# Performance work log

Measured on AMD Instinct MI355X. Metric: run time of the kernel, lower is better.

The kernel has to match this reference:

```python
import jax, jax.numpy as jnp
import numpy as np

B, S, H = 2, 2048, 1024
NUM_HEADS = 16


def setup_inputs() -> dict:
    key = jax.random.key(0)
    ks = jax.random.split(key, 5)
    scale = 1.0 / np.sqrt(H)
    x = jax.random.normal(ks[0], (B, S, H), dtype=jnp.float32)
    W_qkv = jax.random.normal(ks[1], (3 * H, H), dtype=jnp.float32) * scale
    b_qkv = jax.random.normal(ks[2], (3 * H,), dtype=jnp.float32) * 0.02
    W_o = jax.random.normal(ks[3], (H, H), dtype=jnp.float32) * scale
    b_o = jax.random.normal(ks[4], (H,), dtype=jnp.float32) * 0.02
    return {"x": x, "W_qkv": W_qkv, "b_qkv": b_qkv, "W_o": W_o, "b_o": b_o}


def reference(x, W_qkv, b_qkv, W_o, b_o):
    b, s, h = x.shape
    n = NUM_HEADS
    d_head = h // n
    # QKV projection (torch Linear: x @ W.T + b), then chunk into Q, K, V
    qkv = x @ W_qkv.T + b_qkv                      # [b, s, 3h]
    Q, K, V = jnp.split(qkv, 3, axis=-1)           # each [b, s, h]
    # split heads: b s (n d) -> b n s d
    Q = Q.reshape(b, s, n, d_head).transpose(0, 2, 1, 3)
    K = K.reshape(b, s, n, d_head).transpose(0, 2, 1, 3)
    V = V.reshape(b, s, n, d_head).transpose(0, 2, 1, 3)
    # scores, causal mask, scale (mask before/after scale is equivalent: -inf stays -inf)
    scores = jnp.einsum('bnqd,bnkd->bnqk', Q, K) / jnp.sqrt(jnp.float32(d_head))
    causal = jnp.tril(jnp.ones((s, s), dtype=bool))  # True = keep
    scores = jnp.where(causal, scores, -jnp.inf)
    A = jax.nn.softmax(scores, axis=-1)
    AV = jnp.einsum('bnqk,bnkd->bnqd', A, V)
    out = AV.transpose(0, 2, 1, 3).reshape(b, s, h)  # merge heads
    return out @ W_o.T + b_o
```

## Files before the change

kernel.cpp:

```cpp
#include <hip/hip_runtime.h>
#include <cstdint>
#include <cstddef>

#define BATCH 2
#define SEQ   2048
#define HID   1024
#define NHEAD 16
#define DHEAD 64
#define QKV_N 3072
#define NTOK  4096

typedef __attribute__((ext_vector_type(4))) float f32x4;
typedef __attribute__((ext_vector_type(8))) short bf16x8;

#define QSCL 0.18033688011112042f

__device__ inline unsigned short f2bf(float f) {
    union { float f; unsigned int u; } v; v.f = f;
    unsigned int u = v.u;
    unsigned int r = (u + 0x7fffu + ((u >> 16) & 1u)) >> 16;
    return (unsigned short)r;
}

__device__ __forceinline__ unsigned int pack_bf16_rh(float a, float b) {
    union { float f; unsigned int u; } ua, ub;
    ua.f = a; ub.f = b;
    return ((ua.u + 0x8000u) >> 16) | ((ub.u + 0x8000u) & 0xffff0000u);
}

__device__ __forceinline__ void gload_lds16(const void* g, void* l) {
    __builtin_amdgcn_global_load_lds(
        (const __attribute__((address_space(1))) void*)g,
        (__attribute__((address_space(3))) void*)l, 16, 0, 0);
}

__global__ void cast_f32_bf16(const float* __restrict__ in, unsigned short* __restrict__ out, int n4) {
    int i = blockIdx.x * blockDim.x + threadIdx.x;
    if (i >= n4) return;
    float4 v = reinterpret_cast<const float4*>(in)[i];
    ushort4 o;
    o.x = f2bf(v.x); o.y = f2bf(v.y); o.z = f2bf(v.z); o.w = f2bf(v.w);
    reinterpret_cast<ushort4*>(out)[i] = o;
}

template<int BN, int OUT_MODE>
__global__ __launch_bounds__(256) void gemm_bt(const short* __restrict__ A,
                                               const short* __restrict__ B,
                                               const float* __restrict__ bias,
                                               void* __restrict__ Cout,
                                               int M, int N, int K) {
    constexpr int WTN = BN / 2;
    constexpr int NJ  = WTN / 16;
    constexpr int NBC = BN / 64;

    __shared__ short sA[2][128 * 32];
    __shared__ short sB[2][BN * 32];

    const int tid  = threadIdx.x;
    const int lane = tid & 63;
    const int wave = tid >> 6;
    const int wm = wave >> 1, wn = wave & 1;

    const int nwg = gridDim.x;
    const int swz = (blockIdx.x & 7) * (nwg >> 3) + (blockIdx.x >> 3);
    const int tiles_n = N / BN;
    const int m0 = (swz / tiles_n) * 128;
    const int n0 = (swz % tiles_n) * BN;

    f32x4 acc[4][NJ];
    #pragma unroll
    for (int i = 0; i < 4; ++i)
        #pragma unroll
        for (int j = 0; j < NJ; ++j) acc[i][j] = (f32x4){0.f, 0.f, 0.f, 0.f};

    const int r = lane & 15;
    const int G = lane >> 4;

    #define GSTAGE(kt_, buf_)                                                          \
        {                                                                              \
            _Pragma("unroll")                                                          \
            for (int i = 0; i < 2; ++i) {                                              \
                int ga = (i * 4 + wave) * 64 + lane;                                   \
                int row = ga >> 2, gcol = (ga & 3) ^ (row & 3);                        \
                gload_lds16(A + (size_t)(m0 + row) * K + (kt_) + gcol * 8,             \
                            &sA[buf_][(i * 4 + wave) * 512]);                          \
            }                                                                          \
            _Pragma("unroll")                                                          \
            for (int i = 0; i < NBC; ++i) {                                            \
                int gb = (i * 4 + wave) * 64 + lane;                                   \
                int row = gb >> 2, gcol = (gb & 3) ^ (row & 3);                        \
                gload_lds16(B + (size_t)(n0 + row) * K + (kt_) + gcol * 8,             \
                            &sB[buf_][(i * 4 + wave) * 512]);                          \
            }                                                                          \
        }

    GSTAGE(0, 0);
    __syncthreads();
    int cur = 0;

    const int nsteps = K >> 5;
    for (int ks = 0; ks < nsteps; ++ks) {
        if (ks + 1 < nsteps) GSTAGE((ks + 1) * 32, cur ^ 1);

        const int sg = G ^ (r & 3);
        bf16x8 af[4], bfr[NJ];
        #pragma unroll
        for (int i = 0; i < 4; ++i) {
            int row = wm * 64 + i * 16 + r;
            af[i] = *reinterpret_cast<const bf16x8*>(&sA[cur][row * 32 + sg * 8]);
        }
        #pragma unroll
        for (int j = 0; j < NJ; ++j) {
            int row = wn * WTN + j * 16 + r;
            bfr[j] = *reinterpret_cast<const bf16x8*>(&sB[cur][row * 32 + sg * 8]);
        }
        #pragma unroll
        for (int i = 0; i < 4; ++i)
            #pragma unroll
            for (int j = 0; j < NJ; ++j)
                acc[i][j] = __builtin_amdgcn_mfma_f32_16x16x32_bf16(af[i], bfr[j], acc[i][j], 0, 0, 0);

        __syncthreads();
        cur ^= 1;
    }
    #undef GSTAGE

    const int col_l = lane & 15;
    const int row_g = (lane >> 4) * 4;
    #pragma unroll
    for (int i = 0; i < 4; ++i) {
        #pragma unroll
        for (int j = 0; j < NJ; ++j) {
            int nn = n0 + wn * WTN + j * 16 + col_l;
            float bv = bias[nn];
            float scl = (OUT_MODE == 2 && nn < HID) ? QSCL : 1.0f;
            #pragma unroll
            for (int reg = 0; reg < 4; ++reg) {
                int mm = m0 + wm * 64 + i * 16 + row_g + reg;
                float v = (acc[i][j][reg] + bv) * scl;
                if (OUT_MODE == 0) {
                    reinterpret_cast<float*>(Cout)[(size_t)mm * N + nn] = v;
                } else {
                    reinterpret_cast<unsigned short*>(Cout)[(size_t)mm * N + nn] = f2bf(v);
                }
            }
        }
    }
}

#define TLDP 72
__global__ __launch_bounds__(256) void transpose_v(const short* __restrict__ qkv,
                                                   short* __restrict__ vP) {
    const int st = blockIdx.x;
    const int bh = blockIdx.y;
    const int b  = bh >> 4, h = bh & 15;
    __shared__ short ld[64 * TLDP];
    const int tid = threadIdx.x;

    #pragma unroll
    for (int i = 0; i < 2; ++i) {
        int idx = i * 256 + tid;
        int row = idx >> 3, c = idx & 7;
        int4 v = *reinterpret_cast<const int4*>(
            qkv + ((size_t)(b * SEQ + st * 64 + row)) * QKV_N + 2 * HID + h * DHEAD + c * 8);
        *reinterpret_cast<int4*>(&ld[row * TLDP + c * 8]) = v;
    }
    __syncthreads();
    #pragma unroll
    for (int i = 0; i < 2; ++i) {
        int u  = i * 256 + tid;
        int Tp = u >> 8;
        int d  = (u >> 2) & 63;
        int p  = u & 3;
        int b0 = Tp * 32 + 4 * p;
        int b1 = b0 + 16;
        ushort4 o0, o1;
        o0.x = (unsigned short)ld[(b0 + 0) * TLDP + d];
        o0.y = (unsigned short)ld[(b0 + 1) * TLDP + d];
        o0.z = (unsigned short)ld[(b0 + 2) * TLDP + d];
        o0.w = (unsigned short)ld[(b0 + 3) * TLDP + d];
        o1.x = (unsigned short)ld[(b1 + 0) * TLDP + d];
        o1.y = (unsigned short)ld[(b1 + 1) * TLDP + d];
        o1.z = (unsigned short)ld[(b1 + 2) * TLDP + d];
        o1.w = (unsigned short)ld[(b1 + 3) * TLDP + d];
        size_t out = ((size_t)((bh * 64 + st * 2 + Tp) * 64 + d)) * 32 + p * 8;
        *reinterpret_cast<ushort4*>(&vP[out])     = o0;
        *reinterpret_cast<ushort4*>(&vP[out + 4]) = o1;
    }
}

__global__ __launch_bounds__(256) void attn_fwd(const short* __restrict__ qkv,
                                                const short* __restrict__ vP,
                                                short* __restrict__ av) {
    const int bid = blockIdx.x;
    const int qb  = 31 - (bid >> 5);
    const int bh  = bid & 31;
    const int b   = bh >> 4;
    const int h   = bh & 15;

    __shared__ float comb[64][68];

    const int tid  = threadIdx.x;
    const int lane = tid & 63;
    const int wave = tid >> 6;
    const int r    = lane & 15;
    const int G    = lane >> 4;
    const int row_g = G * 4;

    const int qbw = qb * 64;

    bf16x8 qf[4][2];
    #pragma unroll
    for (int mi = 0; mi < 4; ++mi) {
        const short* Qg = qkv + ((size_t)(b * SEQ + qbw + mi * 16 + r)) * QKV_N + h * DHEAD;
        qf[mi][0] = *reinterpret_cast<const bf16x8*>(Qg + G * 8);
        qf[mi][1] = *reinterpret_cast<const bf16x8*>(Qg + 32 + G * 8);
    }

    f32x4 oacc[4][4];
    f32x4 oL[4];
    #pragma unroll
    for (int mi = 0; mi < 4; ++mi) {
        oL[mi] = (f32x4){0.f, 0.f, 0.f, 0.f};
        #pragma unroll
        for (int dg = 0; dg < 4; ++dg) oacc[mi][dg] = (f32x4){0.f, 0.f, 0.f, 0.f};
    }

    bf16x8 ones;
    #pragma unroll
    for (int e = 0; e < 8; ++e) ones[e] = (short)0x3f80;

    const short* kpt = qkv + (size_t)(b * SEQ + wave * 32) * QKV_N + HID + h * DHEAD
                       + r * QKV_N + G * 8;
    const short* vpt = vP + (size_t)(bh * 64 + wave) * 2048 + r * 32 + G * 8;
    const ptrdiff_t KSTEP = (ptrdiff_t)128 * QKV_N;
    const ptrdiff_t VSTEP = 4 * 2048;
    const int KG1 = 16 * QKV_N;

    const int tlast = 2 * qb + 1;
    for (int t = wave; t <= tlast; t += 4) {
        int4 k00 = *reinterpret_cast<const int4*>(kpt);
        int4 k01 = *reinterpret_cast<const int4*>(kpt + 32);
        int4 k10 = *reinterpret_cast<const int4*>(kpt + KG1);
        int4 k11 = *reinterpret_cast<const int4*>(kpt + KG1 + 32);
        int4 v0 = *reinterpret_cast<const int4*>(vpt);
        int4 v1 = *reinterpret_cast<const int4*>(vpt + 16 * 32);
        int4 v2 = *reinterpret_cast<const int4*>(vpt + 32 * 32);
        int4 v3 = *reinterpret_cast<const int4*>(vpt + 48 * 32);
        kpt += KSTEP;
        vpt += VSTEP;

        bf16x8 kb[2][2], vb[4];
        __builtin_memcpy(&kb[0][0], &k00, 16);
        __builtin_memcpy(&kb[0][1], &k01, 16);
        __builtin_memcpy(&kb[1][0], &k10, 16);
        __builtin_memcpy(&kb[1][1], &k11, 16);
        __builtin_memcpy(&vb[0], &v0, 16);
        __builtin_memcpy(&vb[1], &v1, 16);
        __builtin_memcpy(&vb[2], &v2, 16);
        __builtin_memcpy(&vb[3], &v3, 16);

        const bool band = (t >= 2 * qb);

        #pragma unroll
        for (int mi = 0; mi < 4; ++mi) {
            f32x4 s[2];
            #pragma unroll
            for (int g = 0; g < 2; ++g) {
                f32x4 z = (f32x4){0.f, 0.f, 0.f, 0.f};
                z = __builtin_amdgcn_mfma_f32_16x16x32_bf16(kb[g][0], qf[mi][0], z, 0, 0, 0);
                z = __builtin_amdgcn_mfma_f32_16x16x32_bf16(kb[g][1], qf[mi][1], z, 0, 0, 0);
                s[g] = z;
            }
            if (band) {
                int qg = qbw + mi * 16 + r;
                #pragma unroll
                for (int g = 0; g < 2; ++g) {
                    #pragma unroll
                    for (int reg = 0; reg < 4; ++reg) {
                        int kvg = t * 32 + g * 16 + row_g + reg;
                        if (kvg > qg) s[g][reg] = -30000.f;
                    }
                }
            }
            float p0 = __builtin_amdgcn_exp2f(s[0][0]);
            float p1 = __builtin_amdgcn_exp2f(s[0][1]);
            float p2 = __builtin_amdgcn_exp2f(s[0][2]);
            float p3 = __builtin_amdgcn_exp2f(s[0][3]);
            float p4 = __builtin_amdgcn_exp2f(s[1][0]);
            float p5 = __builtin_amdgcn_exp2f(s[1][1]);
            float p6 = __builtin_amdgcn_exp2f(s[1][2]);
            float p7 = __builtin_amdgcn_exp2f(s[1][3]);
            unsigned int w0 = pack_bf16_rh(p0, p1);
            unsigned int w1 = pack_bf16_rh(p2, p3);
            unsigned int w2 = pack_bf16_rh(p4, p5);
            unsigned int w3 = pack_bf16_rh(p6, p7);
            bf16x8 pb;
            { int4 f; f.x = (int)w0; f.y = (int)w1; f.z = (int)w2; f.w = (int)w3;
              __builtin_memcpy(&pb, &f, 16); }

            #pragma unroll
            for (int dg = 0; dg < 4; ++dg)
                oacc[mi][dg] = __builtin_amdgcn_mfma_f32_16x16x32_bf16(vb[dg], pb, oacc[mi][dg], 0, 0, 0);
            oL[mi] = __builtin_amdgcn_mfma_f32_16x16x32_bf16(ones, pb, oL[mi], 0, 0, 0);
        }
    }

    __syncthreads();
    if (wave == 0) {
        #pragma unroll
        for (int mi = 0; mi < 4; ++mi) {
            #pragma unroll
            for (int dg = 0; dg < 4; ++dg)
                *reinterpret_cast<f32x4*>(&comb[mi * 16 + r][dg * 16 + row_g]) = oacc[mi][dg];
            if (G == 0) comb[mi * 16 + r][64] = oL[mi][0];
        }
    }
    __syncthreads();
    if (wave == 1) {
        #pragma unroll
        for (int mi = 0; mi < 4; ++mi) {
            #pragma unroll
            for (int dg = 0; dg < 4; ++dg) {
                f32x4 c = *reinterpret_cast<f32x4*>(&comb[mi * 16 + r][dg * 16 + row_g]);
                *reinterpret_cast<f32x4*>(&comb[mi * 16 + r][dg * 16 + row_g]) = c + oacc[mi][dg];
            }
            if (G == 0) comb[mi * 16 + r][64] += oL[mi][0];
        }
    }
    __syncthreads();
    if (wave == 2) {
        #pragma unroll
        for (int mi = 0; mi < 4; ++mi) {
            #pragma unroll
            for (int dg = 0; dg < 4; ++dg) {
                f32x4 c = *reinterpret_cast<f32x4*>(&comb[mi * 16 + r][dg * 16 + row_g]);
                *reinterpret_cast<f32x4*>(&comb[mi * 16 + r][dg * 16 + row_g]) = c + oacc[mi][dg];
            }
            if (G == 0) comb[mi * 16 + r][64] += oL[mi][0];
        }
    }
    __syncthreads();
    if (wave == 3) {
        #pragma unroll
        for (int mi = 0; mi < 4; ++mi) {
            float l = comb[mi * 16 + r][64] + oL[mi][0];
            float il = 1.0f / l;
            size_t tok = (size_t)(b * SEQ + qbw + mi * 16 + r);
            #pragma unroll
            for (int dg = 0; dg < 4; ++dg) {
                f32x4 tot = *reinterpret_cast<f32x4*>(&comb[mi * 16 + r][dg * 16 + row_g]);
                tot = tot + oacc[mi][dg];
                ushort4 o;
                o.x = f2bf(tot[0] * il);
                o.y = f2bf(tot[1] * il);
                o.z = f2bf(tot[2] * il);
                o.w = f2bf(tot[3] * il);
                *reinterpret_cast<ushort4*>(&av[tok * HID + h * DHEAD + dg * 16 + row_g]) = o;
            }
        }
    }
}

extern "C" void kernel_launch(void* const* d_in, const int* in_sizes, int n_in,
                              void* d_out, int out_size, void* d_ws, size_t ws_size,
                              hipStream_t stream) {
    const float* x     = (const float*)d_in[0];
    const float* W_qkv = (const float*)d_in[1];
    const float* b_qkv = (const float*)d_in[2];
    const float* W_o   = (const float*)d_in[3];
    const float* b_o   = (const float*)d_in[4];
    float* out = (float*)d_out;

    const int n_x    = NTOK * HID;
    const int n_wqkv = QKV_N * HID;
    const int n_wo   = HID * HID;
    const int n_qkv  = NTOK * QKV_N;
    const int n_av   = NTOK * HID;

    short* xb    = (short*)d_ws;
    short* wqkvb = xb + n_x;
    short* wob   = wqkvb + n_wqkv;
    short* qkv   = wob + n_wo;
    short* av    = qkv + n_qkv;
    short* vP    = av + n_av;

    cast_f32_bf16<<<n_x / 1024,    256, 0, stream>>>(x,     (unsigned short*)xb,    n_x / 4);
    cast_f32_bf16<<<n_wqkv / 1024, 256, 0, stream>>>(W_qkv, (unsigned short*)wqkvb, n_wqkv / 4);
    cast_f32_bf16<<<n_wo / 1024,   256, 0, stream>>>(W_o,   (unsigned short*)wob,   n_wo / 4);

    gemm_bt<128, 2><<<(NTOK / 128) * (QKV_N / 128), 256, 0, stream>>>(
        xb, wqkvb, b_qkv, (void*)qkv, NTOK, QKV_N, HID);

    transpose_v<<<dim3(SEQ / 64, BATCH * NHEAD), 256, 0, stream>>>(qkv, vP);

    attn_fwd<<<1024, 256, 0, stream>>>(qkv, vP, av);

    gemm_bt<64, 0><<<(NTOK / 128) * (HID / 64), 256, 0, stream>>>(
        av, wob, b_o, (void*)out, NTOK, HID, HID);
}
```

Measured before the change: 114.7 us.

## Split attention key tiles across eight waves with tree reduction of partials

The attention block grows from 4 to 8 waves, and each wave strides over key tiles by 8 instead of 4, so each query block spreads its key work over more waves. The sequential four-step combine through one shared buffer becomes a tree reduction over four shared buffers (8 to 4 to 2 to 1). The aim is to shorten the per-block serial key loop and the combine chain. The cost is about four times more LDS per block (roughly 70KB) and a 512-thread launch bound, which may limit how many blocks fit on a CU and may raise register pressure.

```diff
diff --git a/kernel.cpp b/kernel.cpp
--- a/kernel.cpp
+++ b/kernel.cpp
@@ -189,7 +189,7 @@
     }
 }
 
-__global__ __launch_bounds__(256) void attn_fwd(const short* __restrict__ qkv,
+__global__ __launch_bounds__(512) void attn_fwd(const short* __restrict__ qkv,
                                                 const short* __restrict__ vP,
                                                 short* __restrict__ av) {
     const int bid = blockIdx.x;
@@ -198,7 +198,7 @@
     const int b   = bh >> 4;
     const int h   = bh & 15;
 
-    __shared__ float comb[64][68];
+    __shared__ float comb[4][64][68];
 
     const int tid  = threadIdx.x;
     const int lane = tid & 63;
@@ -233,12 +233,12 @@
     const short* kpt = qkv + (size_t)(b * SEQ + wave * 32) * QKV_N + HID + h * DHEAD
                        + r * QKV_N + G * 8;
     const short* vpt = vP + (size_t)(bh * 64 + wave) * 2048 + r * 32 + G * 8;
-    const ptrdiff_t KSTEP = (ptrdiff_t)128 * QKV_N;
-    const ptrdiff_t VSTEP = 4 * 2048;
+    const ptrdiff_t KSTEP = (ptrdiff_t)256 * QKV_N;
+    const ptrdiff_t VSTEP = 8 * 2048;
     const int KG1 = 16 * QKV_N;
 
     const int tlast = 2 * qb + 1;
-    for (int t = wave; t <= tlast; t += 4) {
+    for (int t = wave; t <= tlast; t += 8) {
         int4 k00 = *reinterpret_cast<const int4*>(kpt);
         int4 k01 = *reinterpret_cast<const int4*>(kpt + 32);
         int4 k10 = *reinterpret_cast<const int4*>(kpt + KG1);
@@ -306,60 +306,63 @@
         }
     }
 
+    #define CSTORE(bi_)                                                                 \
+        {                                                                               \
+            _Pragma("unroll")                                                           \
+            for (int mi = 0; mi < 4; ++mi) {                                            \
+                _Pragma("unroll")                                                       \
+                for (int dg = 0; dg < 4; ++dg)                                          \
+                    *reinterpret_cast<f32x4*>(&comb[bi_][mi * 16 + r][dg * 16 + row_g]) \
+                        = oacc[mi][dg];                                                 \
+                if (G == 0) comb[bi_][mi * 16 + r][64] = oL[mi][0];                     \
+            }                                                                           \
+        }
+    #define CADD(bi_)                                                                   \
+        {                                                                               \
+            _Pragma("unroll")                                                           \
+            for (int mi = 0; mi < 4; ++mi) {                                            \
+                _Pragma("unroll")                                                       \
+                for (int dg = 0; dg < 4; ++dg) {                                        \
+                    f32x4 c = *reinterpret_cast<f32x4*>(                                \
+                        &comb[bi_][mi * 16 + r][dg * 16 + row_g]);                      \
+                    oacc[mi][dg] = oacc[mi][dg] + c;                                    \
+                }                                                                       \
+                oL[mi][0] += comb[bi_][mi * 16 + r][64];                                \
+            }                                                                           \
+        }
+
+    __syncthreads();
+    if (wave >= 4) CSTORE(wave - 4);
+    __syncthreads();
+    if (wave < 4) {
+        CADD(wave);
+        if (wave >= 2) CSTORE(wave);
+    }
+    __syncthreads();
+    if (wave < 2) {
+        CADD(wave + 2);
+        if (wave == 1) CSTORE(1);
+    }
     __syncthreads();
     if (wave == 0) {
+        CADD(1);
         #pragma unroll
         for (int mi = 0; mi < 4; ++mi) {
-            #pragma unroll
-            for (int dg = 0; dg < 4; ++dg)
-                *reinterpret_cast<f32x4*>(&comb[mi * 16 + r][dg * 16 + row_g]) = oacc[mi][dg];
-            if (G == 0) comb[mi * 16 + r][64] = oL[mi][0];
-        }
-    }
-    __syncthreads();
-    if (wave == 1) {
-        #pragma unroll
-        for (int mi = 0; mi < 4; ++mi) {
-            #pragma unroll
-            for (int dg = 0; dg < 4; ++dg) {
-                f32x4 c = *reinterpret_cast<f32x4*>(&comb[mi * 16 + r][dg * 16 + row_g]);
-                *reinterpret_cast<f32x4*>(&comb[mi * 16 + r][dg * 16 + row_g]) = c + oacc[mi][dg];
-            }
-            if (G == 0) comb[mi * 16 + r][64] += oL[mi][0];
-        }
-    }
-    __syncthreads();
-    if (wave == 2) {
-        #pragma unroll
-        for (int mi = 0; mi < 4; ++mi) {
-            #pragma unroll
-            for (int dg = 0; dg < 4; ++dg) {
-                f32x4 c = *reinterpret_cast<f32x4*>(&comb[mi * 16 + r][dg * 16 + row_g]);
-                *reinterpret_cast<f32x4*>(&comb[mi * 16 + r][dg * 16 + row_g]) = c + oacc[mi][dg];
-            }
-            if (G == 0) comb[mi * 16 + r][64] += oL[mi][0];
-        }
-    }
-    __syncthreads();
-    if (wave == 3) {
-        #pragma unroll
-        for (int mi = 0; mi < 4; ++mi) {
-            float l = comb[mi * 16 + r][64] + oL[mi][0];
-            float il = 1.0f / l;
+            float il = 1.0f / oL[mi][0];
             size_t tok = (size_t)(b * SEQ + qbw + mi * 16 + r);
             #pragma unroll
             for (int dg = 0; dg < 4; ++dg) {
-                f32x4 tot = *reinterpret_cast<f32x4*>(&comb[mi * 16 + r][dg * 16 + row_g]);
-                tot = tot + oacc[mi][dg];
                 ushort4 o;
-                o.x = f2bf(tot[0] * il);
-                o.y = f2bf(tot[1] * il);
-                o.z = f2bf(tot[2] * il);
-                o.w = f2bf(tot[3] * il);
+                o.x = f2bf(oacc[mi][dg][0] * il);
+                o.y = f2bf(oacc[mi][dg][1] * il);
+                o.z = f2bf(oacc[mi][dg][2] * il);
+                o.w = f2bf(oacc[mi][dg][3] * il);
                 *reinterpret_cast<ushort4*>(&av[tok * HID + h * DHEAD + dg * 16 + row_g]) = o;
             }
         }
     }
+    #undef CSTORE
+    #undef CADD
 }
 
 extern "C" void kernel_launch(void* const* d_in, const int* in_sizes, int n_in,
@@ -394,7 +397,7 @@
 
     transpose_v<<<dim3(SEQ / 64, BATCH * NHEAD), 256, 0, stream>>>(qkv, vP);
 
-    attn_fwd<<<1024, 256, 0, stream>>>(qkv, vP, av);
+    attn_fwd<<<1024, 512, 0, stream>>>(qkv, vP, av);
 
     gemm_bt<64, 0><<<(NTOK / 128) * (HID / 64), 256, 0, stream>>>(
         av, wob, b_o, (void*)out, NTOK, HID, HID);
```

Measured after the change: 126.9 us. 1.11x slower.

## Pair causal query blocks per workgroup, prefetch K/V, and raise MFMA priority

Applied to the files above, without the earlier changes.

Each attention workgroup now processes two query blocks, a long one (31-pi) and a short one (pi), so every block does the same causal work and the grid drops to 512 blocks. The K/V loads for the next tile are issued before the current tile's MFMAs to hide global-memory latency. s_setprio raises wave priority around the MFMA sections, and launch bounds request 2 blocks per CU. The costs are higher register pressure from the prefetch buffers and fewer blocks in flight to hide latency.

```diff
diff --git a/kernel.cpp b/kernel.cpp
--- a/kernel.cpp
+++ b/kernel.cpp
@@ -189,11 +189,11 @@
     }
 }
 
-__global__ __launch_bounds__(256) void attn_fwd(const short* __restrict__ qkv,
-                                                const short* __restrict__ vP,
-                                                short* __restrict__ av) {
+__global__ __launch_bounds__(256, 2) void attn_fwd(const short* __restrict__ qkv,
+                                                   const short* __restrict__ vP,
+                                                   short* __restrict__ av) {
     const int bid = blockIdx.x;
-    const int qb  = 31 - (bid >> 5);
+    const int pi  = bid >> 5;
     const int bh  = bid & 31;
     const int b   = bh >> 4;
     const int h   = bh & 15;
@@ -207,158 +207,184 @@
     const int G    = lane >> 4;
     const int row_g = G * 4;
 
-    const int qbw = qb * 64;
-
-    bf16x8 qf[4][2];
-    #pragma unroll
-    for (int mi = 0; mi < 4; ++mi) {
-        const short* Qg = qkv + ((size_t)(b * SEQ + qbw + mi * 16 + r)) * QKV_N + h * DHEAD;
-        qf[mi][0] = *reinterpret_cast<const bf16x8*>(Qg + G * 8);
-        qf[mi][1] = *reinterpret_cast<const bf16x8*>(Qg + 32 + G * 8);
-    }
-
-    f32x4 oacc[4][4];
-    f32x4 oL[4];
-    #pragma unroll
-    for (int mi = 0; mi < 4; ++mi) {
-        oL[mi] = (f32x4){0.f, 0.f, 0.f, 0.f};
-        #pragma unroll
-        for (int dg = 0; dg < 4; ++dg) oacc[mi][dg] = (f32x4){0.f, 0.f, 0.f, 0.f};
-    }
-
     bf16x8 ones;
     #pragma unroll
     for (int e = 0; e < 8; ++e) ones[e] = (short)0x3f80;
 
-    const short* kpt = qkv + (size_t)(b * SEQ + wave * 32) * QKV_N + HID + h * DHEAD
-                       + r * QKV_N + G * 8;
-    const short* vpt = vP + (size_t)(bh * 64 + wave) * 2048 + r * 32 + G * 8;
+    const short* kpt0 = qkv + (size_t)(b * SEQ + wave * 32) * QKV_N + HID + h * DHEAD
+                        + r * QKV_N + G * 8;
+    const short* vpt0 = vP + (size_t)(bh * 64 + wave) * 2048 + r * 32 + G * 8;
     const ptrdiff_t KSTEP = (ptrdiff_t)128 * QKV_N;
     const ptrdiff_t VSTEP = 4 * 2048;
     const int KG1 = 16 * QKV_N;
 
-    const int tlast = 2 * qb + 1;
-    for (int t = wave; t <= tlast; t += 4) {
-        int4 k00 = *reinterpret_cast<const int4*>(kpt);
-        int4 k01 = *reinterpret_cast<const int4*>(kpt + 32);
-        int4 k10 = *reinterpret_cast<const int4*>(kpt + KG1);
-        int4 k11 = *reinterpret_cast<const int4*>(kpt + KG1 + 32);
-        int4 v0 = *reinterpret_cast<const int4*>(vpt);
-        int4 v1 = *reinterpret_cast<const int4*>(vpt + 16 * 32);
-        int4 v2 = *reinterpret_cast<const int4*>(vpt + 32 * 32);
-        int4 v3 = *reinterpret_cast<const int4*>(vpt + 48 * 32);
-        kpt += KSTEP;
-        vpt += VSTEP;
-
-        bf16x8 kb[2][2], vb[4];
-        __builtin_memcpy(&kb[0][0], &k00, 16);
-        __builtin_memcpy(&kb[0][1], &k01, 16);
-        __builtin_memcpy(&kb[1][0], &k10, 16);
-        __builtin_memcpy(&kb[1][1], &k11, 16);
-        __builtin_memcpy(&vb[0], &v0, 16);
-        __builtin_memcpy(&vb[1], &v1, 16);
-        __builtin_memcpy(&vb[2], &v2, 16);
-        __builtin_memcpy(&vb[3], &v3, 16);
-
-        const bool band = (t >= 2 * qb);
-
+    #pragma unroll 1
+    for (int job = 0; job < 2; ++job) {
+        const int qb  = job == 0 ? 31 - pi : pi;
+        const int qbw = qb * 64;
+
+        bf16x8 qf[4][2];
         #pragma unroll
         for (int mi = 0; mi < 4; ++mi) {
-            f32x4 s[2];
-            #pragma unroll
-            for (int g = 0; g < 2; ++g) {
-                f32x4 z = (f32x4){0.f, 0.f, 0.f, 0.f};
-                z = __builtin_amdgcn_mfma_f32_16x16x32_bf16(kb[g][0], qf[mi][0], z, 0, 0, 0);
-                z = __builtin_amdgcn_mfma_f32_16x16x32_bf16(kb[g][1], qf[mi][1], z, 0, 0, 0);
-                s[g] = z;
-            }
-            if (band) {
-                int qg = qbw + mi * 16 + r;
+            const short* Qg = qkv + ((size_t)(b * SEQ + qbw + mi * 16 + r)) * QKV_N + h * DHEAD;
+            qf[mi][0] = *reinterpret_cast<const bf16x8*>(Qg + G * 8);
+            qf[mi][1] = *reinterpret_cast<const bf16x8*>(Qg + 32 + G * 8);
+        }
+
+        f32x4 oacc[4][4];
+        f32x4 oL[4];
+        #pragma unroll
+        for (int mi = 0; mi < 4; ++mi) {
+            oL[mi] = (f32x4){0.f, 0.f, 0.f, 0.f};
+            #pragma unroll
+            for (int dg = 0; dg < 4; ++dg) oacc[mi][dg] = (f32x4){0.f, 0.f, 0.f, 0.f};
+        }
+
+        const short* kpt = kpt0;
+        const short* vpt = vpt0;
+        const int tlast = 2 * qb + 1;
+
+        int4 kc00 = *reinterpret_cast<const int4*>(kpt);
+        int4 kc01 = *reinterpret_cast<const int4*>(kpt + 32);
+        int4 kc10 = *reinterpret_cast<const int4*>(kpt + KG1);
+        int4 kc11 = *reinterpret_cast<const int4*>(kpt + KG1 + 32);
+        int4 vc0  = *reinterpret_cast<const int4*>(vpt);
+        int4 vc1  = *reinterpret_cast<const int4*>(vpt + 16 * 32);
+        int4 vc2  = *reinterpret_cast<const int4*>(vpt + 32 * 32);
+        int4 vc3  = *reinterpret_cast<const int4*>(vpt + 48 * 32);
+
+        for (int t = wave; t <= tlast; t += 4) {
+            const bool more = (t + 4 <= tlast);
+            const short* kn = more ? kpt + KSTEP : kpt;
+            const short* vn = more ? vpt + VSTEP : vpt;
+            int4 kn00 = *reinterpret_cast<const int4*>(kn);
+            int4 kn01 = *reinterpret_cast<const int4*>(kn + 32);
+            int4 kn10 = *reinterpret_cast<const int4*>(kn + KG1);
+            int4 kn11 = *reinterpret_cast<const int4*>(kn + KG1 + 32);
+            int4 vn0  = *reinterpret_cast<const int4*>(vn);
+            int4 vn1  = *reinterpret_cast<const int4*>(vn + 16 * 32);
+            int4 vn2  = *reinterpret_cast<const int4*>(vn + 32 * 32);
+            int4 vn3  = *reinterpret_cast<const int4*>(vn + 48 * 32);
+            kpt = kn; vpt = vn;
+
+            bf16x8 kb[2][2], vb[4];
+            __builtin_memcpy(&kb[0][0], &kc00, 16);
+            __builtin_memcpy(&kb[0][1], &kc01, 16);
+            __builtin_memcpy(&kb[1][0], &kc10, 16);
+            __builtin_memcpy(&kb[1][1], &kc11, 16);
+            __builtin_memcpy(&vb[0], &vc0, 16);
+            __builtin_memcpy(&vb[1], &vc1, 16);
+            __builtin_memcpy(&vb[2], &vc2, 16);
+            __builtin_memcpy(&vb[3], &vc3, 16);
+
+            const bool band = (t >= 2 * qb);
+
+            #pragma unroll
+            for (int mi = 0; mi < 4; ++mi) {
+                f32x4 s[2];
+                __builtin_amdgcn_s_setprio(1);
                 #pragma unroll
                 for (int g = 0; g < 2; ++g) {
+                    f32x4 z = (f32x4){0.f, 0.f, 0.f, 0.f};
+                    z = __builtin_amdgcn_mfma_f32_16x16x32_bf16(kb[g][0], qf[mi][0], z, 0, 0, 0);
+                    z = __builtin_amdgcn_mfma_f32_16x16x32_bf16(kb[g][1], qf[mi][1], z, 0, 0, 0);
+                    s[g] = z;
+                }
+                __builtin_amdgcn_s_setprio(0);
+                if (band) {
+                    int qg = qbw + mi * 16 + r;
                     #pragma unroll
-                    for (int reg = 0; reg < 4; ++reg) {
-                        int kvg = t * 32 + g * 16 + row_g + reg;
-                        if (kvg > qg) s[g][reg] = -30000.f;
+                    for (int g = 0; g < 2; ++g) {
+                        #pragma unroll
+                        for (int reg = 0; reg < 4; ++reg) {
+                            int kvg = t * 32 + g * 16 + row_g + reg;
+                            if (kvg > qg) s[g][reg] = -30000.f;
+                        }
                     }
                 }
-            }
-            float p0 = __builtin_amdgcn_exp2f(s[0][0]);
-            float p1 = __builtin_amdgcn_exp2f(s[0][1]);
-            float p2 = __builtin_amdgcn_exp2f(s[0][2]);
-            float p3 = __builtin_amdgcn_exp2f(s[0][3]);
-            float p4 = __builtin_amdgcn_exp2f(s[1][0]);
-            float p5 = __builtin_amdgcn_exp2f(s[1][1]);
-            float p6 = __builtin_amdgcn_exp2f(s[1][2]);
-            float p7 = __builtin_amdgcn_exp2f(s[1][3]);
-            unsigned int w0 = pack_bf16_rh(p0, p1);
-            unsigned int w1 = pack_bf16_rh(p2, p3);
-            unsigned int w2 = pack_bf16_rh(p4, p5);
-            unsigned int w3 = pack_bf16_rh(p6, p7);
-            bf16x8 pb;
-            { int4 f; f.x = (int)w0; f.y = (int)w1; f.z = (int)w2; f.w = (int)w3;
-              __builtin_memcpy(&pb, &f, 16); }
-
-            #pragma unroll
-            for (int dg = 0; dg < 4; ++dg)
-                oacc[mi][dg] = __builtin_amdgcn_mfma_f32_16x16x32_bf16(vb[dg], pb, oacc[mi][dg], 0, 0, 0);
-            oL[mi] = __builtin_amdgcn_mfma_f32_16x16x32_bf16(ones, pb, oL[mi], 0, 0, 0);
-        }
-    }
-
-    __syncthreads();
-    if (wave == 0) {
-        #pragma unroll
-        for (int mi = 0; mi < 4; ++mi) {
-            #pragma unroll
-            for (int dg = 0; dg < 4; ++dg)
-                *reinterpret_cast<f32x4*>(&comb[mi * 16 + r][dg * 16 + row_g]) = oacc[mi][dg];
-            if (G == 0) comb[mi * 16 + r][64] = oL[mi][0];
-        }
-    }
-    __syncthreads();
-    if (wave == 1) {
-        #pragma unroll
-        for (int mi = 0; mi < 4; ++mi) {
-            #pragma unroll
-            for (int dg = 0; dg < 4; ++dg) {
-                f32x4 c = *reinterpret_cast<f32x4*>(&comb[mi * 16 + r][dg * 16 + row_g]);
-                *reinterpret_cast<f32x4*>(&comb[mi * 16 + r][dg * 16 + row_g]) = c + oacc[mi][dg];
-            }
-            if (G == 0) comb[mi * 16 + r][64] += oL[mi][0];
-        }
-    }
-    __syncthreads();
-    if (wave == 2) {
-        #pragma unroll
-        for (int mi = 0; mi < 4; ++mi) {
-            #pragma unroll
-            for (int dg = 0; dg < 4; ++dg) {
-                f32x4 c = *reinterpret_cast<f32x4*>(&comb[mi * 16 + r][dg * 16 + row_g]);
-                *reinterpret_cast<f32x4*>(&comb[mi * 16 + r][dg * 16 + row_g]) = c + oacc[mi][dg];
-            }
-            if (G == 0) comb[mi * 16 + r][64] += oL[mi][0];
-        }
-    }
-    __syncthreads();
-    if (wave == 3) {
-        #pragma unroll
-        for (int mi = 0; mi < 4; ++mi) {
-            float l = comb[mi * 16 + r][64] + oL[mi][0];
-            float il = 1.0f / l;
-            size_t tok = (size_t)(b * SEQ + qbw + mi * 16 + r);
-            #pragma unroll
-            for (int dg = 0; dg < 4; ++dg) {
-                f32x4 tot = *reinterpret_cast<f32x4*>(&comb[mi * 16 + r][dg * 16 + row_g]);
-                tot = tot + oacc[mi][dg];
-                ushort4 o;
-                o.x = f2bf(tot[0] * il);
-                o.y = f2bf(tot[1] * il);
-                o.z = f2bf(tot[2] * il);
-                o.w = f2bf(tot[3] * il);
-                *reinterpret_cast<ushort4*>(&av[tok * HID + h * DHEAD + dg * 16 + row_g]) = o;
-            }
-        }
+                float p0 = __builtin_amdgcn_exp2f(s[0][0]);
+                float p1 = __builtin_amdgcn_exp2f(s[0][1]);
+                float p2 = __builtin_amdgcn_exp2f(s[0][2]);
+                float p3 = __builtin_amdgcn_exp2f(s[0][3]);
+                float p4 = __builtin_amdgcn_exp2f(s[1][0]);
+                float p5 = __builtin_amdgcn_exp2f(s[1][1]);
+                float p6 = __builtin_amdgcn_exp2f(s[1][2]);
+                float p7 = __builtin_amdgcn_exp2f(s[1][3]);
+                unsigned int w0 = pack_bf16_rh(p0, p1);
+                unsigned int w1 = pack_bf16_rh(p2, p3);
+                unsigned int w2 = pack_bf16_rh(p4, p5);
+                unsigned int w3 = pack_bf16_rh(p6, p7);
+                bf16x8 pb;
+                { int4 f; f.x = (int)w0; f.y = (int)w1; f.z = (int)w2; f.w = (int)w3;
+                  __builtin_memcpy(&pb, &f, 16); }
+
+                __builtin_amdgcn_s_setprio(1);
+                #pragma unroll
+                for (int dg = 0; dg < 4; ++dg)
+                    oacc[mi][dg] = __builtin_amdgcn_mfma_f32_16x16x32_bf16(vb[dg], pb, oacc[mi][dg], 0, 0, 0);
+                oL[mi] = __builtin_amdgcn_mfma_f32_16x16x32_bf16(ones, pb, oL[mi], 0, 0, 0);
+                __builtin_amdgcn_s_setprio(0);
+            }
+
+            kc00 = kn00; kc01 = kn01; kc10 = kn10; kc11 = kn11;
+            vc0 = vn0; vc1 = vn1; vc2 = vn2; vc3 = vn3;
+        }
+
+        __syncthreads();
+        if (wave == 0) {
+            #pragma unroll
+            for (int mi = 0; mi < 4; ++mi) {
+                #pragma unroll
+                for (int dg = 0; dg < 4; ++dg)
+                    *reinterpret_cast<f32x4*>(&comb[mi * 16 + r][dg * 16 + row_g]) = oacc[mi][dg];
+                if (G == 0) comb[mi * 16 + r][64] = oL[mi][0];
+            }
+        }
+        __syncthreads();
+        if (wave == 1) {
+            #pragma unroll
+            for (int mi = 0; mi < 4; ++mi) {
+                #pragma unroll
+                for (int dg = 0; dg < 4; ++dg) {
+                    f32x4 c = *reinterpret_cast<f32x4*>(&comb[mi * 16 + r][dg * 16 + row_g]);
+                    *reinterpret_cast<f32x4*>(&comb[mi * 16 + r][dg * 16 + row_g]) = c + oacc[mi][dg];
+                }
+                if (G == 0) comb[mi * 16 + r][64] += oL[mi][0];
+            }
+        }
+        __syncthreads();
+        if (wave == 2) {
+            #pragma unroll
+            for (int mi = 0; mi < 4; ++mi) {
+                #pragma unroll
+                for (int dg = 0; dg < 4; ++dg) {
+                    f32x4 c = *reinterpret_cast<f32x4*>(&comb[mi * 16 + r][dg * 16 + row_g]);
+                    *reinterpret_cast<f32x4*>(&comb[mi * 16 + r][dg * 16 + row_g]) = c + oacc[mi][dg];
+                }
+                if (G == 0) comb[mi * 16 + r][64] += oL[mi][0];
+            }
+        }
+        __syncthreads();
+        if (wave == 3) {
+            #pragma unroll
+            for (int mi = 0; mi < 4; ++mi) {
+                float l = comb[mi * 16 + r][64] + oL[mi][0];
+                float il = 1.0f / l;
+                size_t tok = (size_t)(b * SEQ + qbw + mi * 16 + r);
+                #pragma unroll
+                for (int dg = 0; dg < 4; ++dg) {
+                    f32x4 tot = *reinterpret_cast<f32x4*>(&comb[mi * 16 + r][dg * 16 + row_g]);
+                    tot = tot + oacc[mi][dg];
+                    ushort4 o;
+                    o.x = f2bf(tot[0] * il);
+                    o.y = f2bf(tot[1] * il);
+                    o.z = f2bf(tot[2] * il);
+                    o.w = f2bf(tot[3] * il);
+                    *reinterpret_cast<ushort4*>(&av[tok * HID + h * DHEAD + dg * 16 + row_g]) = o;
+                }
+            }
+        }
+        __syncthreads();
     }
 }
 
@@ -394,7 +420,7 @@
 
     transpose_v<<<dim3(SEQ / 64, BATCH * NHEAD), 256, 0, stream>>>(qkv, vP);
 
-    attn_fwd<<<1024, 256, 0, stream>>>(qkv, vP, av);
+    attn_fwd<<<512, 256, 0, stream>>>(qkv, vP, av);
 
     gemm_bt<64, 0><<<(NTOK / 128) * (HID / 64), 256, 0, stream>>>(
         av, wob, b_o, (void*)out, NTOK, HID, HID);
```

Measured after the change: 114.6 us. About the same (-0.1%).

## Pair causal query blocks per workgroup and double KV tiles per iteration

Applied to the files above, without the earlier changes.

Each attention workgroup now handles two query blocks, a long one (31-pi) and a short one (pi), so every block does a balanced amount of causal work, and the grid is halved to 512. The inner loop loads two 32-row K/V subtiles per iteration to raise memory-level parallelism, adds s_setprio around the MFMA sections, and sets launch_bounds to 2 blocks per CU. This trades the tail imbalance of the causal triangle for longer-lived blocks, higher register pressure from the doubled loads, and an extra cross-wave reduction per block.

```diff
diff --git a/kernel.cpp b/kernel.cpp
--- a/kernel.cpp
+++ b/kernel.cpp
@@ -189,11 +189,11 @@
     }
 }
 
-__global__ __launch_bounds__(256) void attn_fwd(const short* __restrict__ qkv,
-                                                const short* __restrict__ vP,
-                                                short* __restrict__ av) {
+__global__ __launch_bounds__(256, 2) void attn_fwd(const short* __restrict__ qkv,
+                                                   const short* __restrict__ vP,
+                                                   short* __restrict__ av) {
     const int bid = blockIdx.x;
-    const int qb  = 31 - (bid >> 5);
+    const int pi  = bid >> 5;
     const int bh  = bid & 31;
     const int b   = bh >> 4;
     const int h   = bh & 15;
@@ -207,159 +207,184 @@
     const int G    = lane >> 4;
     const int row_g = G * 4;
 
-    const int qbw = qb * 64;
-
-    bf16x8 qf[4][2];
-    #pragma unroll
-    for (int mi = 0; mi < 4; ++mi) {
-        const short* Qg = qkv + ((size_t)(b * SEQ + qbw + mi * 16 + r)) * QKV_N + h * DHEAD;
-        qf[mi][0] = *reinterpret_cast<const bf16x8*>(Qg + G * 8);
-        qf[mi][1] = *reinterpret_cast<const bf16x8*>(Qg + 32 + G * 8);
-    }
-
-    f32x4 oacc[4][4];
-    f32x4 oL[4];
-    #pragma unroll
-    for (int mi = 0; mi < 4; ++mi) {
-        oL[mi] = (f32x4){0.f, 0.f, 0.f, 0.f};
-        #pragma unroll
-        for (int dg = 0; dg < 4; ++dg) oacc[mi][dg] = (f32x4){0.f, 0.f, 0.f, 0.f};
-    }
-
     bf16x8 ones;
     #pragma unroll
     for (int e = 0; e < 8; ++e) ones[e] = (short)0x3f80;
 
-    const short* kpt = qkv + (size_t)(b * SEQ + wave * 32) * QKV_N + HID + h * DHEAD
-                       + r * QKV_N + G * 8;
-    const short* vpt = vP + (size_t)(bh * 64 + wave) * 2048 + r * 32 + G * 8;
-    const ptrdiff_t KSTEP = (ptrdiff_t)128 * QKV_N;
-    const ptrdiff_t VSTEP = 4 * 2048;
+    const short* kpt0 = qkv + (size_t)(b * SEQ + wave * 64) * QKV_N + HID + h * DHEAD
+                        + r * QKV_N + G * 8;
+    const short* vpt0 = vP + (size_t)(bh * 64 + wave * 2) * 2048 + r * 32 + G * 8;
+    const ptrdiff_t KSTEP = (ptrdiff_t)256 * QKV_N;
+    const ptrdiff_t VSTEP = 8 * 2048;
     const int KG1 = 16 * QKV_N;
-
-    const int tlast = 2 * qb + 1;
-    for (int t = wave; t <= tlast; t += 4) {
-        int4 k00 = *reinterpret_cast<const int4*>(kpt);
-        int4 k01 = *reinterpret_cast<const int4*>(kpt + 32);
-        int4 k10 = *reinterpret_cast<const int4*>(kpt + KG1);
-        int4 k11 = *reinterpret_cast<const int4*>(kpt + KG1 + 32);
-        int4 v0 = *reinterpret_cast<const int4*>(vpt);
-        int4 v1 = *reinterpret_cast<const int4*>(vpt + 16 * 32);
-        int4 v2 = *reinterpret_cast<const int4*>(vpt + 32 * 32);
-        int4 v3 = *reinterpret_cast<const int4*>(vpt + 48 * 32);
-        kpt += KSTEP;
-        vpt += VSTEP;
-
-        bf16x8 kb[2][2], vb[4];
-        __builtin_memcpy(&kb[0][0], &k00, 16);
-        __builtin_memcpy(&kb[0][1], &k01, 16);
-        __builtin_memcpy(&kb[1][0], &k10, 16);
-        __builtin_memcpy(&kb[1][1], &k11, 16);
-        __builtin_memcpy(&vb[0], &v0, 16);
-        __builtin_memcpy(&vb[1], &v1, 16);
-        __builtin_memcpy(&vb[2], &v2, 16);
-        __builtin_memcpy(&vb[3], &v3, 16);
-
-        const bool band = (t >= 2 * qb);
-
+    const int KH  = 32 * QKV_N;
+
+    #define SUBTILE(K00_, K01_, K10_, K11_, V0_, V1_, V2_, V3_, TG_)                       \
+        {                                                                                  \
+            bf16x8 kb[2][2], vb[4];                                                        \
+            __builtin_memcpy(&kb[0][0], &K00_, 16);                                        \
+            __builtin_memcpy(&kb[0][1], &K01_, 16);                                        \
+            __builtin_memcpy(&kb[1][0], &K10_, 16);                                        \
+            __builtin_memcpy(&kb[1][1], &K11_, 16);                                        \
+            __builtin_memcpy(&vb[0], &V0_, 16);                                            \
+            __builtin_memcpy(&vb[1], &V1_, 16);                                            \
+            __builtin_memcpy(&vb[2], &V2_, 16);                                            \
+            __builtin_memcpy(&vb[3], &V3_, 16);                                            \
+            _Pragma("unroll")                                                              \
+            for (int mi = 0; mi < 4; ++mi) {                                               \
+                f32x4 s[2];                                                                \
+                __builtin_amdgcn_s_setprio(1);                                             \
+                _Pragma("unroll")                                                          \
+                for (int g = 0; g < 2; ++g) {                                              \
+                    f32x4 z = (f32x4){0.f, 0.f, 0.f, 0.f};                                 \
+                    z = __builtin_amdgcn_mfma_f32_16x16x32_bf16(kb[g][0], qf[mi][0], z, 0, 0, 0); \
+                    z = __builtin_amdgcn_mfma_f32_16x16x32_bf16(kb[g][1], qf[mi][1], z, 0, 0, 0); \
+                    s[g] = z;                                                              \
+                }                                                                          \
+                __builtin_amdgcn_s_setprio(0);                                             \
+                if (band) {                                                                \
+                    int qg = qbw + mi * 16 + r;                                            \
+                    _Pragma("unroll")                                                      \
+                    for (int g = 0; g < 2; ++g) {                                          \
+                        _Pragma("unroll")                                                  \
+                        for (int reg = 0; reg < 4; ++reg) {                                \
+                            int kvg = (TG_) * 32 + g * 16 + row_g + reg;                   \
+                            if (kvg > qg) s[g][reg] = -30000.f;                            \
+                        }                                                                  \
+                    }                                                                      \
+                }                                                                          \
+                float p0 = __builtin_amdgcn_exp2f(s[0][0]);                                \
+                float p1 = __builtin_amdgcn_exp2f(s[0][1]);                                \
+                float p2 = __builtin_amdgcn_exp2f(s[0][2]);                                \
+                float p3 = __builtin_amdgcn_exp2f(s[0][3]);                                \
+                float p4 = __builtin_amdgcn_exp2f(s[1][0]);                                \
+                float p5 = __builtin_amdgcn_exp2f(s[1][1]);                                \
+                float p6 = __builtin_amdgcn_exp2f(s[1][2]);                                \
+                float p7 = __builtin_amdgcn_exp2f(s[1][3]);                                \
+                unsigned int w0 = pack_bf16_rh(p0, p1);                                    \
+                unsigned int w1 = pack_bf16_rh(p2, p3);                                    \
+                unsigned int w2 = pack_bf16_rh(p4, p5);                                    \
+                unsigned int w3 = pack_bf16_rh(p6, p7);                                    \
+                bf16x8 pb;                                                                 \
+                { int4 f; f.x = (int)w0; f.y = (int)w1; f.z = (int)w2; f.w = (int)w3;      \
+                  __builtin_memcpy(&pb, &f, 16); }                                         \
+                __builtin_amdgcn_s_setprio(1);                                             \
+                _Pragma("unroll")                                                          \
+                for (int dg = 0; dg < 4; ++dg)                                             \
+                    oacc[mi][dg] = __builtin_amdgcn_mfma_f32_16x16x32_bf16(vb[dg], pb, oacc[mi][dg], 0, 0, 0); \
+                oL[mi] = __builtin_amdgcn_mfma_f32_16x16x32_bf16(ones, pb, oL[mi], 0, 0, 0); \
+                __builtin_amdgcn_s_setprio(0);                                             \
+            }                                                                              \
+        }
+
+    #pragma unroll 1
+    for (int job = 0; job < 2; ++job) {
+        const int qb  = job == 0 ? 31 - pi : pi;
+        const int qbw = qb * 64;
+
+        bf16x8 qf[4][2];
         #pragma unroll
         for (int mi = 0; mi < 4; ++mi) {
-            f32x4 s[2];
-            #pragma unroll
-            for (int g = 0; g < 2; ++g) {
-                f32x4 z = (f32x4){0.f, 0.f, 0.f, 0.f};
-                z = __builtin_amdgcn_mfma_f32_16x16x32_bf16(kb[g][0], qf[mi][0], z, 0, 0, 0);
-                z = __builtin_amdgcn_mfma_f32_16x16x32_bf16(kb[g][1], qf[mi][1], z, 0, 0, 0);
-                s[g] = z;
+            const short* Qg = qkv + ((size_t)(b * SEQ + qbw + mi * 16 + r)) * QKV_N + h * DHEAD;
+            qf[mi][0] = *reinterpret_cast<const bf16x8*>(Qg + G * 8);
+            qf[mi][1] = *reinterpret_cast<const bf16x8*>(Qg + 32 + G * 8);
+        }
+
+        f32x4 oacc[4][4];
+        f32x4 oL[4];
+        #pragma unroll
+        for (int mi = 0; mi < 4; ++mi) {
+            oL[mi] = (f32x4){0.f, 0.f, 0.f, 0.f};
+            #pragma unroll
+            for (int dg = 0; dg < 4; ++dg) oacc[mi][dg] = (f32x4){0.f, 0.f, 0.f, 0.f};
+        }
+
+        const short* kpt = kpt0;
+        const short* vpt = vpt0;
+
+        for (int tp = wave; tp <= qb; tp += 4) {
+            int4 ka00 = *reinterpret_cast<const int4*>(kpt);
+            int4 ka01 = *reinterpret_cast<const int4*>(kpt + 32);
+            int4 ka10 = *reinterpret_cast<const int4*>(kpt + KG1);
+            int4 ka11 = *reinterpret_cast<const int4*>(kpt + KG1 + 32);
+            int4 kb00 = *reinterpret_cast<const int4*>(kpt + KH);
+            int4 kb01 = *reinterpret_cast<const int4*>(kpt + KH + 32);
+            int4 kb10 = *reinterpret_cast<const int4*>(kpt + KH + KG1);
+            int4 kb11 = *reinterpret_cast<const int4*>(kpt + KH + KG1 + 32);
+            int4 va0 = *reinterpret_cast<const int4*>(vpt);
+            int4 va1 = *reinterpret_cast<const int4*>(vpt + 16 * 32);
+            int4 va2 = *reinterpret_cast<const int4*>(vpt + 32 * 32);
+            int4 va3 = *reinterpret_cast<const int4*>(vpt + 48 * 32);
+            int4 vb0 = *reinterpret_cast<const int4*>(vpt + 2048);
+            int4 vb1 = *reinterpret_cast<const int4*>(vpt + 2048 + 16 * 32);
+            int4 vb2 = *reinterpret_cast<const int4*>(vpt + 2048 + 32 * 32);
+            int4 vb3 = *reinterpret_cast<const int4*>(vpt + 2048 + 48 * 32);
+            kpt += KSTEP;
+            vpt += VSTEP;
+
+            const bool band = (tp == qb);
+
+            SUBTILE(ka00, ka01, ka10, ka11, va0, va1, va2, va3, 2 * tp);
+            SUBTILE(kb00, kb01, kb10, kb11, vb0, vb1, vb2, vb3, 2 * tp + 1);
+        }
+
+        __syncthreads();
+        if (wave == 0) {
+            #pragma unroll
+            for (int mi = 0; mi < 4; ++mi) {
+                #pragma unroll
+                for (int dg = 0; dg < 4; ++dg)
+                    *reinterpret_cast<f32x4*>(&comb[mi * 16 + r][dg * 16 + row_g]) = oacc[mi][dg];
+                if (G == 0) comb[mi * 16 + r][64] = oL[mi][0];
             }
-            if (band) {
-                int qg = qbw + mi * 16 + r;
+        }
+        __syncthreads();
+        if (wave == 1) {
+            #pragma unroll
+            for (int mi = 0; mi < 4; ++mi) {
                 #pragma unroll
-                for (int g = 0; g < 2; ++g) {
-                    #pragma unroll
-                    for (int reg = 0; reg < 4; ++reg) {
-                        int kvg = t * 32 + g * 16 + row_g + reg;
-                        if (kvg > qg) s[g][reg] = -30000.f;
-                    }
+                for (int dg = 0; dg < 4; ++dg) {
+                    f32x4 c = *reinterpret_cast<f32x4*>(&comb[mi * 16 + r][dg * 16 + row_g]);
+                    *reinterpret_cast<f32x4*>(&comb[mi * 16 + r][dg * 16 + row_g]) = c + oacc[mi][dg];
+                }
+                if (G == 0) comb[mi * 16 + r][64] += oL[mi][0];
+            }
+        }
+        __syncthreads();
+        if (wave == 2) {
+            #pragma unroll
+            for (int mi = 0; mi < 4; ++mi) {
+                #pragma unroll
+                for (int dg = 0; dg < 4; ++dg) {
+                    f32x4 c = *reinterpret_cast<f32x4*>(&comb[mi * 16 + r][dg * 16 + row_g]);
+                    *reinterpret_cast<f32x4*>(&comb[mi * 16 + r][dg * 16 + row_g]) = c + oacc[mi][dg];
+                }
+                if (G == 0) comb[mi * 16 + r][64] += oL[mi][0];
+            }
+        }
+        __syncthreads();
+        if (wave == 3) {
+            #pragma unroll
+            for (int mi = 0; mi < 4; ++mi) {
+                float l = comb[mi * 16 + r][64] + oL[mi][0];
+                float il = 1.0f / l;
+                size_t tok = (size_t)(b * SEQ + qbw + mi * 16 + r);
+                #pragma unroll
+                for (int dg = 0; dg < 4; ++dg) {
+                    f32x4 tot = *reinterpret_cast<f32x4*>(&comb[mi * 16 + r][dg * 16 + row_g]);
+                    tot = tot + oacc[mi][dg];
+                    ushort4 o;
+                    o.x = f2bf(tot[0] * il);
+                    o.y = f2bf(tot[1] * il);
+                    o.z = f2bf(tot[2] * il);
+                    o.w = f2bf(tot[3] * il);
+                    *reinterpret_cast<ushort4*>(&av[tok * HID + h * DHEAD + dg * 16 + row_g]) = o;
                 }
             }
-            float p0 = __builtin_amdgcn_exp2f(s[0][0]);
-            float p1 = __builtin_amdgcn_exp2f(s[0][1]);
-            float p2 = __builtin_amdgcn_exp2f(s[0][2]);
-            float p3 = __builtin_amdgcn_exp2f(s[0][3]);
-            float p4 = __builtin_amdgcn_exp2f(s[1][0]);
-            float p5 = __builtin_amdgcn_exp2f(s[1][1]);
-            float p6 = __builtin_amdgcn_exp2f(s[1][2]);
-            float p7 = __builtin_amdgcn_exp2f(s[1][3]);
-            unsigned int w0 = pack_bf16_rh(p0, p1);
-            unsigned int w1 = pack_bf16_rh(p2, p3);
-            unsigned int w2 = pack_bf16_rh(p4, p5);
-            unsigned int w3 = pack_bf16_rh(p6, p7);
-            bf16x8 pb;
-            { int4 f; f.x = (int)w0; f.y = (int)w1; f.z = (int)w2; f.w = (int)w3;
-              __builtin_memcpy(&pb, &f, 16); }
-
-            #pragma unroll
-            for (int dg = 0; dg < 4; ++dg)
-                oacc[mi][dg] = __builtin_amdgcn_mfma_f32_16x16x32_bf16(vb[dg], pb, oacc[mi][dg], 0, 0, 0);
-            oL[mi] = __builtin_amdgcn_mfma_f32_16x16x32_bf16(ones, pb, oL[mi], 0, 0, 0);
-        }
+        }
+        __syncthreads();
     }
-
-    __syncthreads();
-    if (wave == 0) {
-        #pragma unroll
-        for (int mi = 0; mi < 4; ++mi) {
-            #pragma unroll
-            for (int dg = 0; dg < 4; ++dg)
-                *reinterpret_cast<f32x4*>(&comb[mi * 16 + r][dg * 16 + row_g]) = oacc[mi][dg];
-            if (G == 0) comb[mi * 16 + r][64] = oL[mi][0];
-        }
-    }
-    __syncthreads();
-    if (wave == 1) {
-        #pragma unroll
-        for (int mi = 0; mi < 4; ++mi) {
-            #pragma unroll
-            for (int dg = 0; dg < 4; ++dg) {
-                f32x4 c = *reinterpret_cast<f32x4*>(&comb[mi * 16 + r][dg * 16 + row_g]);
-                *reinterpret_cast<f32x4*>(&comb[mi * 16 + r][dg * 16 + row_g]) = c + oacc[mi][dg];
-            }
-            if (G == 0) comb[mi * 16 + r][64] += oL[mi][0];
-        }
-    }
-    __syncthreads();
-    if (wave == 2) {
-        #pragma unroll
-        for (int mi = 0; mi < 4; ++mi) {
-            #pragma unroll
-            for (int dg = 0; dg < 4; ++dg) {
-                f32x4 c = *reinterpret_cast<f32x4*>(&comb[mi * 16 + r][dg * 16 + row_g]);
-                *reinterpret_cast<f32x4*>(&comb[mi * 16 + r][dg * 16 + row_g]) = c + oacc[mi][dg];
-            }
-            if (G == 0) comb[mi * 16 + r][64] += oL[mi][0];
-        }
-    }
-    __syncthreads();
-    if (wave == 3) {
-        #pragma unroll
-        for (int mi = 0; mi < 4; ++mi) {
-            float l = comb[mi * 16 + r][64] + oL[mi][0];
-            float il = 1.0f / l;
-            size_t tok = (size_t)(b * SEQ + qbw + mi * 16 + r);
-            #pragma unroll
-            for (int dg = 0; dg < 4; ++dg) {
-                f32x4 tot = *reinterpret_cast<f32x4*>(&comb[mi * 16 + r][dg * 16 + row_g]);
-                tot = tot + oacc[mi][dg];
-                ushort4 o;
-                o.x = f2bf(tot[0] * il);
-                o.y = f2bf(tot[1] * il);
-                o.z = f2bf(tot[2] * il);
-                o.w = f2bf(tot[3] * il);
-                *reinterpret_cast<ushort4*>(&av[tok * HID + h * DHEAD + dg * 16 + row_g]) = o;
-            }
-        }
-    }
+    #undef SUBTILE
 }
 
 extern "C" void kernel_launch(void* const* d_in, const int* in_sizes, int n_in,
@@ -394,7 +419,7 @@
 
     transpose_v<<<dim3(SEQ / 64, BATCH * NHEAD), 256, 0, stream>>>(qkv, vP);
 
-    attn_fwd<<<1024, 256, 0, stream>>>(qkv, vP, av);
+    attn_fwd<<<512, 256, 0, stream>>>(qkv, vP, av);
 
     gemm_bt<64, 0><<<(NTOK / 128) * (HID / 64), 256, 0, stream>>>(
         av, wob, b_o, (void*)out, NTOK, HID, HID);
```

Result: no change. 113.6 us (-0.9%).
